# Kernel tuning notes

Measured on AMD Instinct MI355X. Metric: run time of the kernel, lower is better.

The kernel has to match this reference:

```python
import jax, jax.numpy as jnp
import numpy as np

EPS = 1e-5

def _bn(x, g, b):
    # training-mode BatchNorm1d: per-feature batch stats (biased var), affine
    mu = jnp.mean(x, 0)
    var = jnp.var(x, 0)
    return (x - mu) * jax.lax.rsqrt(var + EPS) * g + b

def _sage(x_src, x_dst, src, dst, Wl, bl, Wr):
    # PyG SAGEConv(mean): lin_l(mean_{j in N(i)} x_j) + lin_r(x_i); lin_r has no bias
    n = x_dst.shape[0]
    s = jax.ops.segment_sum(x_src[src], dst, num_segments=n)          # [N_dst, H]
    c = jax.ops.segment_sum(jnp.ones(src.shape, x_src.dtype), dst, num_segments=n)
    m = s / jnp.maximum(c, 1.0)[:, None]                              # mean aggregation; isolated nodes -> 0
    return m @ Wl + bl + x_dst @ Wr


def setup_inputs() -> dict:
    ND, NG, NS = 30000, 60000, 15000
    FD, FG, FS = 256, 128, 64
    H, O = 128, 64
    E = dict(dg=500000, gd=500000, gs=400000, sg=400000, ds=150000, sd=150000)
    keys = iter(jax.random.split(jax.random.key(0), 64))
    def nrm(shape, s=0.05):
        return jax.random.normal(next(keys), shape, jnp.float32) * s
    def ridx(n, hi):
        return jax.random.randint(next(keys), (n,), 0, hi, jnp.int32)
    inp = {
        'x_drug': nrm((ND, FD), 1.0), 'x_gene': nrm((NG, FG), 1.0), 'x_dis': nrm((NS, FS), 1.0),
        'src_dg': ridx(E['dg'], ND), 'dst_dg': ridx(E['dg'], NG),
        'src_gd': ridx(E['gd'], NG), 'dst_gd': ridx(E['gd'], ND),
        'src_gs': ridx(E['gs'], NG), 'dst_gs': ridx(E['gs'], NS),
        'src_sg': ridx(E['sg'], NS), 'dst_sg': ridx(E['sg'], NG),
        'src_ds': ridx(E['ds'], ND), 'dst_ds': ridx(E['ds'], NS),
        'src_sd': ridx(E['sd'], NS), 'dst_sd': ridx(E['sd'], ND),
        # input projections per node type
        'W_in_drug': nrm((FD, H)), 'b_in_drug': jnp.zeros((H,), jnp.float32),
        'W_in_gene': nrm((FG, H)), 'b_in_gene': jnp.zeros((H,), jnp.float32),
        'W_in_dis':  nrm((FS, H)), 'b_in_dis':  jnp.zeros((H,), jnp.float32),
        # input norms, [3 node types, H]
        'g_in': jnp.ones((3, H), jnp.float32), 'bt_in': jnp.zeros((3, H), jnp.float32),
        # SAGEConv weights: [3 layers, 6 edge types, H, H]; order: dg,gd,gs,sg,ds,sd
        'Wl': nrm((3, 6, H, H)), 'Wr': nrm((3, 6, H, H)), 'bl': jnp.zeros((3, 6, H), jnp.float32),
        # per-layer per-type norms [3 layers, 3 types, H]
        'g_conv': jnp.ones((3, 3, H), jnp.float32), 'bt_conv': jnp.zeros((3, 3, H), jnp.float32),
        'W_fin': nrm((H, O)), 'b_fin': jnp.zeros((O,), jnp.float32),
    }
    return inp


def reference(x_drug, x_gene, x_dis,
              src_dg, dst_dg, src_gd, dst_gd, src_gs, dst_gs,
              src_sg, dst_sg, src_ds, dst_ds, src_sd, dst_sd,
              W_in_drug, b_in_drug, W_in_gene, b_in_gene, W_in_dis, b_in_dis,
              g_in, bt_in, Wl, Wr, bl, g_conv, bt_conv, W_fin, b_fin):
    relu = jax.nn.relu
    # input proj + BN + ReLU (dropout in eval mode = identity)
    hd = relu(_bn(x_drug @ W_in_drug + b_in_drug, g_in[0], bt_in[0]))
    hg = relu(_bn(x_gene @ W_in_gene + b_in_gene, g_in[1], bt_in[1]))
    hs = relu(_bn(x_dis  @ W_in_dis  + b_in_dis,  g_in[2], bt_in[2]))
    for L in range(3):
        rd, rg, rs = hd, hg, hs
        # HeteroConv aggr='mean' over the two edge types hitting each dst type
        od = ( _sage(rg, rd, src_gd, dst_gd, Wl[L,1], bl[L,1], Wr[L,1])
             + _sage(rs, rd, src_sd, dst_sd, Wl[L,5], bl[L,5], Wr[L,5]) ) * 0.5
        og = ( _sage(rd, rg, src_dg, dst_dg, Wl[L,0], bl[L,0], Wr[L,0])
             + _sage(rs, rg, src_sg, dst_sg, Wl[L,3], bl[L,3], Wr[L,3]) ) * 0.5
        os_ = ( _sage(rg, rs, src_gs, dst_gs, Wl[L,2], bl[L,2], Wr[L,2])
              + _sage(rd, rs, src_ds, dst_ds, Wl[L,4], bl[L,4], Wr[L,4]) ) * 0.5
        hd = relu(_bn(od,  g_conv[L,0], bt_conv[L,0])) + rd
        hg = relu(_bn(og,  g_conv[L,1], bt_conv[L,1])) + rg
        hs = relu(_bn(os_, g_conv[L,2], bt_conv[L,2])) + rs
    return (hd @ W_fin + b_fin, hg @ W_fin + b_fin, hs @ W_fin + b_fin)
```

## Files before the change

### kernel.cpp

```cpp
#include <hip/hip_runtime.h>
#include <cstddef>
#include <cstdint>

typedef _Float16 f16;
typedef _Float16 f16x8 __attribute__((ext_vector_type(8)));
typedef float f32x4 __attribute__((ext_vector_type(4)));

constexpr int ND = 30000, NG = 60000, NS = 15000;
constexpr float BN_EPS = 1e-5f;
constexpr int NBUCK = 64;
constexpr int TBUCK = 6 * NBUCK;
constexpr int PCHUNK = 4096;

static inline int cdiv(int a, int b){ return (a + b - 1) / b; }


struct BDesc {
    const int* src[6]; const int* dst[6];
    int Ebase[7]; int shift[6]; int N[6];
    int* bCnt; int* bBase; int* bCursor;
    uint2* packed;
    int* offs[6]; int* csr[6];
};

__global__ __launch_bounds__(256) void bhist_k(BDesc bd){
    __shared__ int hist[TBUCK];
    int tid = threadIdx.x;
    for (int i = tid; i < TBUCK; i += 256) hist[i] = 0;
    __syncthreads();
    int Etot = bd.Ebase[6];
    #pragma unroll
    for (int u = 0; u < 16; u++){
        int e = blockIdx.x * PCHUNK + u * 256 + tid;
        if (e < Etot){
            int t = 0;
            #pragma unroll
            for (int i = 1; i < 6; i++) if (e >= bd.Ebase[i]) t = i;
            int d = bd.dst[t][e - bd.Ebase[t]];
            atomicAdd(&hist[t * NBUCK + (d >> bd.shift[t])], 1);
        }
    }
    __syncthreads();
    for (int i = tid; i < TBUCK; i += 256)
        if (hist[i]) atomicAdd(&bd.bCnt[i], hist[i]);
}

__global__ __launch_bounds__(512) void bscan_k(BDesc bd){
    __shared__ int sh[TBUCK];
    int tid = threadIdx.x;
    int my = (tid < TBUCK) ? bd.bCnt[tid] : 0;
    if (tid < TBUCK) sh[tid] = my;
    __syncthreads();
    for (int d = 1; d < TBUCK; d <<= 1){
        int v = (tid < TBUCK) ? sh[tid] : 0;
        int add = (tid >= d && tid < TBUCK) ? sh[tid - d] : 0;
        __syncthreads();
        if (tid < TBUCK) sh[tid] = v + add;
        __syncthreads();
    }
    if (tid < TBUCK){
        int excl = sh[tid] - my;
        bd.bBase[tid] = excl;
        bd.bCursor[tid] = excl;
    }
    if (tid == 0) bd.bBase[TBUCK] = sh[TBUCK - 1];
}

__global__ __launch_bounds__(256) void bpart_k(BDesc bd){
    __shared__ int hist[TBUCK];
    __shared__ int basesh[TBUCK];
    int tid = threadIdx.x;
    for (int i = tid; i < TBUCK; i += 256) hist[i] = 0;
    __syncthreads();
    int Etot = bd.Ebase[6];
    int mb[16], mr[16], ms[16], md[16];
    #pragma unroll
    for (int u = 0; u < 16; u++){
        int e = blockIdx.x * PCHUNK + u * 256 + tid;
        mb[u] = -1;
        if (e < Etot){
            int t = 0;
            #pragma unroll
            for (int i = 1; i < 6; i++) if (e >= bd.Ebase[i]) t = i;
            int le = e - bd.Ebase[t];
            int s = bd.src[t][le], d = bd.dst[t][le];
            int b = t * NBUCK + (d >> bd.shift[t]);
            mr[u] = atomicAdd(&hist[b], 1);
            mb[u] = b; ms[u] = s; md[u] = d;
        }
    }
    __syncthreads();
    for (int i = tid; i < TBUCK; i += 256)
        basesh[i] = hist[i] ? atomicAdd(&bd.bCursor[i], hist[i]) : 0;
    __syncthreads();
    #pragma unroll
    for (int u = 0; u < 16; u++){
        if (mb[u] >= 0){
            int pos = basesh[mb[u]] + mr[u];
            bd.packed[pos] = make_uint2((unsigned)ms[u], (unsigned)md[u]);
        }
    }
}

__global__ __launch_bounds__(256) void bucketCsr_k(BDesc bd){
    __shared__ int cnt[1024];
    __shared__ int sh[256];
    int b = blockIdx.x;
    int t = b >> 6;
    int bb = b & 63;
    int tid = threadIdx.x;
    int shift = bd.shift[t];
    int nodeBase = bb << shift;
    int Nt = bd.N[t];
    int span = 1 << shift;
    int tbase = bd.bBase[t * NBUCK];
    int eBeg = bd.bBase[b], eEnd = bd.bBase[b + 1];
    int bLocal = eBeg - tbase;
    #pragma unroll
    for (int i = 0; i < 4; i++) cnt[tid + i * 256] = 0;
    __syncthreads();
    for (int e = eBeg + tid; e < eEnd; e += 256)
        atomicAdd(&cnt[(int)bd.packed[e].y - nodeBase], 1);
    __syncthreads();
    int c0 = cnt[tid * 4], c1 = cnt[tid * 4 + 1], c2 = cnt[tid * 4 + 2], c3 = cnt[tid * 4 + 3];
    int s = c0 + c1 + c2 + c3;
    sh[tid] = s;
    __syncthreads();
    for (int d = 1; d < 256; d <<= 1){
        int v = sh[tid];
        int add = (tid >= d) ? sh[tid - d] : 0;
        __syncthreads();
        sh[tid] = v + add;
        __syncthreads();
    }
    int run = sh[tid] - s;
    int idx = tid * 4;
    int ex0 = run, ex1 = run + c0, ex2 = ex1 + c1, ex3 = ex2 + c2;
    if (idx     < span && nodeBase + idx     < Nt) bd.offs[t][nodeBase + idx]     = bLocal + ex0;
    if (idx + 1 < span && nodeBase + idx + 1 < Nt) bd.offs[t][nodeBase + idx + 1] = bLocal + ex1;
    if (idx + 2 < span && nodeBase + idx + 2 < Nt) bd.offs[t][nodeBase + idx + 2] = bLocal + ex2;
    if (idx + 3 < span && nodeBase + idx + 3 < Nt) bd.offs[t][nodeBase + idx + 3] = bLocal + ex3;
    cnt[idx] = ex0; cnt[idx + 1] = ex1; cnt[idx + 2] = ex2; cnt[idx + 3] = ex3;
    __syncthreads();
    for (int e = eBeg + tid; e < eEnd; e += 256){
        uint2 p = bd.packed[e];
        int lpos = atomicAdd(&cnt[(int)p.y - nodeBase], 1);
        bd.csr[t][bLocal + lpos] = (int)p.x;
    }
    if (bb == NBUCK - 1 && tid == 0)
        bd.offs[t][Nt] = bd.bBase[(t + 1) * NBUCK] - tbase;
}


struct WDesc {
    const float* W_in0; const float* W_in1; const float* W_in2;
    const float* W_fin; const float* Wl; const float* Wr;
    f16* Wint0; f16* Wint1; f16* Wint2; f16* Wfin_t; f16* Wcat_t;
};

__global__ __launch_bounds__(256) void weightAll_k(WDesc wd){
    int idx = blockIdx.x * 256 + threadIdx.x;
    if (idx < 32768){
        int c = idx >> 8, k = idx & 255;
        wd.Wint0[idx] = (f16)wd.W_in0[k * 128 + c];
    } else if (idx < 49152){
        int l = idx - 32768; int c = l >> 7, k = l & 127;
        wd.Wint1[l] = (f16)wd.W_in1[k * 128 + c];
    } else if (idx < 57344){
        int l = idx - 49152; int c = l >> 6, k = l & 63;
        wd.Wint2[l] = (f16)wd.W_in2[k * 128 + c];
    } else if (idx < 65536){
        int l = idx - 57344; int c = l >> 7, k = l & 127;
        wd.Wfin_t[l] = (f16)wd.W_fin[k * 64 + c];
    } else if (idx < 507904){
        int l = idx - 65536;
        int g = l / (384 * 128);
        int rem = l - g * (384 * 128);
        int c = rem / 384;
        int k = rem - c * 384;
        int L = g / 3, t = g - L * 3;
        const int e1s[3] = {1, 0, 2}, e2s[3] = {5, 3, 4};
        int e1 = e1s[t], e2 = e2s[t];
        float v;
        if (k < 128)      v = wd.Wl[(((size_t)L * 6 + e1) * 128 + k) * 128 + c];
        else if (k < 256) v = wd.Wl[(((size_t)L * 6 + e2) * 128 + (k - 128)) * 128 + c];
        else {
            int kr = k - 256;
            v = wd.Wr[(((size_t)L * 6 + e1) * 128 + kr) * 128 + c]
              + wd.Wr[(((size_t)L * 6 + e2) * 128 + kr) * 128 + c];
        }
        wd.Wcat_t[l] = (f16)v;
    }
}


struct GSeg { const int* offs; const int* csr; const uint4* h; uint4* A; int colPair4; int N; int base; };
struct GDesc { GSeg s[6]; const uint4* zrow; };

__device__ __forceinline__ f16x8 as_h8(uint4 v){
    union { uint4 u; f16x8 h; } c; c.u = v; return c.h;
}

__global__ __launch_bounds__(256) void gatherall_k(GDesc gd){
    int bid = blockIdx.x;
    int si = 0;
    #pragma unroll
    for (int t = 1; t < 6; t++) if (bid >= gd.s[t].base) si = t;
    GSeg sg = gd.s[si];
    int node = (bid - sg.base) * 16 + (threadIdx.x >> 4);
    if (node >= sg.N) return;
    int li = threadIdx.x & 15;
    int s = sg.offs[node], e = sg.offs[node + 1];
    const int* cp = sg.csr;
    const uint4* hp = sg.h;
    const uint4* zr = gd.zrow;
    f16x8 a = {};
    for (int j = s; j < e; j += 8){
        const uint4* p0 = (j + 0 < e) ? (hp + (size_t)cp[j + 0] * 16) : zr;
        const uint4* p1 = (j + 1 < e) ? (hp + (size_t)cp[j + 1] * 16) : zr;
        const uint4* p2 = (j + 2 < e) ? (hp + (size_t)cp[j + 2] * 16) : zr;
        const uint4* p3 = (j + 3 < e) ? (hp + (size_t)cp[j + 3] * 16) : zr;
        const uint4* p4 = (j + 4 < e) ? (hp + (size_t)cp[j + 4] * 16) : zr;
        const uint4* p5 = (j + 5 < e) ? (hp + (size_t)cp[j + 5] * 16) : zr;
        const uint4* p6 = (j + 6 < e) ? (hp + (size_t)cp[j + 6] * 16) : zr;
        const uint4* p7 = (j + 7 < e) ? (hp + (size_t)cp[j + 7] * 16) : zr;
        uint4 v0 = p0[li], v1 = p1[li], v2 = p2[li], v3 = p3[li];
        uint4 v4 = p4[li], v5 = p5[li], v6 = p6[li], v7 = p7[li];
        a = a + as_h8(v0); a = a + as_h8(v1); a = a + as_h8(v2); a = a + as_h8(v3);
        a = a + as_h8(v4); a = a + as_h8(v5); a = a + as_h8(v6); a = a + as_h8(v7);
    }
    float inv = (e > s) ? 1.0f / (float)(e - s) : 0.f;
    union { uint4 u; f16 h[8]; } pk;
    #pragma unroll
    for (int i = 0; i < 8; i++) pk.h[i] = (f16)((float)a[i] * inv);
    sg.A[(size_t)node * 32 + sg.colPair4 + li] = pk.u;
}


struct GemmSeg {
    const f16* A1; const f16* A2; const f16* Wt;
    const float* b1; const float* b2; void* out; float* stats;
    int lda1, lda2, ksplit, N, K, tileBase; float scale;
};
struct GemmDesc { GemmSeg s[3]; };

template<int BN, bool STATS, bool OUT16, bool A32>
__global__ __launch_bounds__(256) void gemmAll_k(GemmDesc gd){
    constexpr int CF = BN / 16;
    __shared__ f16 As[128 * 64];
    __shared__ f16 Bs[BN * 64];
    __shared__ float ssum[BN];
    __shared__ float ssq[BN];
    int bid = blockIdx.x;
    int si = 0;
    #pragma unroll
    for (int t = 1; t < 3; t++) if (bid >= gd.s[t].tileBase) si = t;
    GemmSeg sg = gd.s[si];
    int tid = threadIdx.x;
    int wv = tid >> 6, lane = tid & 63;
    int row0 = (bid - sg.tileBase) * 128;
    int N = sg.N, K = sg.K;
    if (STATS && tid < BN){ ssum[tid] = 0.f; ssq[tid] = 0.f; }

    int rsub = lane >> 3;
    int seg  = lane & 7;
    int sseg = seg ^ rsub;

    f32x4 acc[2][CF];
    #pragma unroll
    for (int rf = 0; rf < 2; rf++)
        #pragma unroll
        for (int cf = 0; cf < CF; cf++)
            acc[rf][cf] = (f32x4){0.f, 0.f, 0.f, 0.f};

    for (int k0 = 0; k0 < K; k0 += 64){
        if (A32){
            const float* Af = (const float*)sg.A1;
            int lda = sg.lda1;
            #pragma unroll
            for (int p = 0; p < 4; p++){
                int sidx = tid + p * 256;
                int r = sidx >> 3, sg8 = sidx & 7;
                int gr = row0 + r;
                int gseg = sg8 ^ (r & 7);
                float4 u0 = make_float4(0.f, 0.f, 0.f, 0.f), u1 = u0;
                if (gr < N){
                    const float* ap = Af + (size_t)gr * lda + k0 + gseg * 8;
                    u0 = *reinterpret_cast<const float4*>(ap);
                    u1 = *reinterpret_cast<const float4*>(ap + 4);
                }
                union { uint4 u; f16 h[8]; } pk;
                pk.h[0] = (f16)u0.x; pk.h[1] = (f16)u0.y; pk.h[2] = (f16)u0.z; pk.h[3] = (f16)u0.w;
                pk.h[4] = (f16)u1.x; pk.h[5] = (f16)u1.y; pk.h[6] = (f16)u1.z; pk.h[7] = (f16)u1.w;
                *reinterpret_cast<uint4*>(&As[r * 64 + sg8 * 8]) = pk.u;
            }
        } else {
            const f16* Ab; int lda, kloc;
            if (k0 < sg.ksplit){ Ab = sg.A1; lda = sg.lda1; kloc = k0; }
            else               { Ab = sg.A2; lda = sg.lda2; kloc = k0 - sg.ksplit; }
            #pragma unroll
            for (int p = 0; p < 4; p++){
                int r = wv * 32 + p * 8 + rsub;
                const f16* srca = Ab + (size_t)(row0 + r) * lda + kloc + sseg * 8;
                __builtin_amdgcn_global_load_lds(
                    (const __attribute__((address_space(1))) void*)srca,
                    (__attribute__((address_space(3))) void*)&As[(wv * 32 + p * 8) * 64],
                    16, 0, 0);
            }
        }
        #pragma unroll
        for (int p = 0; p < BN / 32; p++){
            int c0 = wv * (BN / 4) + p * 8;
            const f16* srcb = sg.Wt + (size_t)(c0 + rsub) * K + k0 + sseg * 8;
            __builtin_amdgcn_global_load_lds(
                (const __attribute__((address_space(1))) void*)srcb,
                (__attribute__((address_space(3))) void*)&Bs[c0 * 64],
                16, 0, 0);
        }
        __syncthreads();
        #pragma unroll
        for (int kf = 0; kf < 2; kf++){
            int kidx = kf * 4 + (lane >> 4);
            int ar0 = wv * 32 + (lane & 15);
            int ar1 = ar0 + 16;
            f16x8 a0 = *reinterpret_cast<const f16x8*>(&As[ar0 * 64 + ((kidx ^ (ar0 & 7)) * 8)]);
            f16x8 a1 = *reinterpret_cast<const f16x8*>(&As[ar1 * 64 + ((kidx ^ (ar1 & 7)) * 8)]);
            #pragma unroll
            for (int cf = 0; cf < CF; cf++){
                int bc = cf * 16 + (lane & 15);
                f16x8 b = *reinterpret_cast<const f16x8*>(&Bs[bc * 64 + ((kidx ^ (bc & 7)) * 8)]);
                acc[0][cf] = __builtin_amdgcn_mfma_f32_16x16x32_f16(a0, b, acc[0][cf], 0, 0, 0);
                acc[1][cf] = __builtin_amdgcn_mfma_f32_16x16x32_f16(a1, b, acc[1][cf], 0, 0, 0);
            }
        }
        __syncthreads();
    }
    int rbase = row0 + wv * 32 + ((lane >> 4) << 2);
    #pragma unroll
    for (int cf = 0; cf < CF; cf++){
        int col = cf * 16 + (lane & 15);
        float bias = 0.f;
        if (sg.b1) bias += sg.b1[col];
        if (sg.b2) bias += sg.b2[col];
        float ls = 0.f, lq = 0.f;
        #pragma unroll
        for (int rf = 0; rf < 2; rf++){
            #pragma unroll
            for (int q = 0; q < 4; q++){
                int gr = rbase + rf * 16 + q;
                if (gr < N){
                    float v = sg.scale * (acc[rf][cf][q] + bias);
                    if (OUT16) ((f16*)sg.out)[(size_t)gr * BN + col] = (f16)v;
                    else       ((float*)sg.out)[(size_t)gr * BN + col] = v;
                    ls += v; lq += v * v;
                }
            }
        }
        if (STATS){ atomicAdd(&ssum[col], ls); atomicAdd(&ssq[col], lq); }
    }
    if (STATS){
        __syncthreads();
        if (tid < BN){
            atomicAdd(&sg.stats[tid], ssum[tid]);
            atomicAdd(&sg.stats[128 + tid], ssq[tid]);
        }
    }
}


struct BnSeg { const f16* o; const float* stats; const float* g; const float* b; f16* h; int N; float invN; int residual; int idxBase; };
struct BnDesc { BnSeg s[3]; int total; };

__global__ __launch_bounds__(256) void bnAll_k(BnDesc bd){
    int idx = blockIdx.x * 256 + threadIdx.x;
    if (idx >= bd.total) return;
    int si = 0;
    #pragma unroll
    for (int t = 1; t < 3; t++) if (idx >= bd.s[t].idxBase) si = t;
    BnSeg sg = bd.s[si];
    int l = idx - sg.idxBase;
    int n = l >> 4, c8 = (l & 15) * 8;
    union { uint4 u; f16 h[8]; } ov;
    ov.u = *reinterpret_cast<const uint4*>(sg.o + (size_t)n * 128 + c8);
    float r[8];
    #pragma unroll
    for (int j = 0; j < 8; j++){
        int c = c8 + j;
        float mu  = sg.stats[c] * sg.invN;
        float var = sg.stats[128 + c] * sg.invN - mu * mu;
        float v = ((float)ov.h[j] - mu) * rsqrtf(var + BN_EPS) * sg.g[c] + sg.b[c];
        r[j] = v > 0.f ? v : 0.f;
    }
    f16* hp = sg.h + (size_t)n * 128 + c8;
    if (sg.residual){
        uint4 old = *reinterpret_cast<const uint4*>(hp);
        union { uint4 u; f16 h[8]; } ou; ou.u = old;
        #pragma unroll
        for (int j = 0; j < 8; j++) r[j] += (float)ou.h[j];
    }
    union { uint4 u; f16 h[8]; } pk;
    #pragma unroll
    for (int j = 0; j < 8; j++) pk.h[j] = (f16)r[j];
    *reinterpret_cast<uint4*>(hp) = pk.u;
}


extern "C" void kernel_launch(void* const* d_in, const int* in_sizes, int n_in,
                              void* d_out, int out_size, void* d_ws, size_t ws_size,
                              hipStream_t stream){
    const float* x_drug = (const float*)d_in[0];
    const float* x_gene = (const float*)d_in[1];
    const float* x_dis  = (const float*)d_in[2];
    const int* srcP[6] = {(const int*)d_in[3], (const int*)d_in[5], (const int*)d_in[7],
                          (const int*)d_in[9], (const int*)d_in[11], (const int*)d_in[13]};
    const int* dstP[6] = {(const int*)d_in[4], (const int*)d_in[6], (const int*)d_in[8],
                          (const int*)d_in[10], (const int*)d_in[12], (const int*)d_in[14]};
    const int  Et[6]   = {in_sizes[3], in_sizes[5], in_sizes[7], in_sizes[9], in_sizes[11], in_sizes[13]};
    const float* W_in[3] = {(const float*)d_in[15], (const float*)d_in[17], (const float*)d_in[19]};
    const float* b_in[3] = {(const float*)d_in[16], (const float*)d_in[18], (const float*)d_in[20]};
    const float* g_in  = (const float*)d_in[21];
    const float* bt_in = (const float*)d_in[22];
    const float* Wl    = (const float*)d_in[23];
    const float* Wr    = (const float*)d_in[24];
    const float* bl    = (const float*)d_in[25];
    const float* g_conv  = (const float*)d_in[26];
    const float* bt_conv = (const float*)d_in[27];
    const float* W_fin = (const float*)d_in[28];
    const float* b_fin = (const float*)d_in[29];
    float* out = (float*)d_out;

    const int Ndst_t[6]     = {NG, ND, NS, NG, NS, ND};
    const int srcT[6]       = {0, 1, 1, 2, 0, 2};
    const int dstT[6]       = {1, 0, 2, 1, 2, 0};
    const int colPair4_t[6] = {0, 0, 0, 16, 16, 16};

    const int Nn[3]  = {ND, NG, NS};
    const int Kin[3] = {256, 128, 64};
    const float* xin[3] = {x_drug, x_gene, x_dis};

    char* base = (char*)d_ws;
    size_t off = 0;
    auto alloc = [&](size_t bytes) -> char* {
        char* p = base + off; off += (bytes + 255) & ~(size_t)255; return p;
    };
    f16* h[3];  for (int t = 0; t < 3; t++) h[t]  = (f16*)alloc((size_t)Nn[t] * 128 * 2);
    f16* A[3];  for (int t = 0; t < 3; t++) A[t]  = (f16*)alloc((size_t)Nn[t] * 256 * 2);
    f16* Wint[3]; for (int t = 0; t < 3; t++) Wint[t] = (f16*)alloc((size_t)128 * Kin[t] * 2);
    f16* Wfin_t = (f16*)alloc((size_t)64 * 128 * 2);
    f16* Wcat_t = (f16*)alloc((size_t)9 * 128 * 384 * 2);
    char* oPool = alloc((size_t)(ND + NG + NS) * 128 * 2);
    f16* o[3];
    o[0] = (f16*)oPool; o[1] = o[0] + (size_t)ND * 128; o[2] = o[1] + (size_t)NG * 128;
    uint2* packed = (uint2*)oPool;
    float* stats = (float*)alloc(12 * 256 * 4);
    int* zeroPool = (int*)alloc((size_t)(TBUCK + 64) * 4);
    int* bCnt = zeroPool;
    const uint4* zrow = (const uint4*)(zeroPool + TBUCK);
    int* bBase   = (int*)alloc((TBUCK + 1) * 4);
    int* bCursor = (int*)alloc(TBUCK * 4);
    int *offs[6], *csr[6];
    for (int t = 0; t < 6; t++) offs[t] = (int*)alloc((size_t)(Ndst_t[t] + 1) * 4);
    for (int t = 0; t < 6; t++) csr[t]  = (int*)alloc((size_t)Et[t] * 4);

    hipMemsetAsync(zeroPool, 0, (size_t)(TBUCK + 64) * 4, stream);
    hipMemsetAsync(stats, 0, 12 * 256 * 4, stream);

    BDesc bd;
    {
        int ecum = 0;
        for (int t = 0; t < 6; t++){
            bd.src[t] = srcP[t]; bd.dst[t] = dstP[t];
            bd.Ebase[t] = ecum; ecum += Et[t];
            int sft = 0; while (((Ndst_t[t] - 1) >> sft) >= NBUCK) sft++;
            bd.shift[t] = sft;
            bd.N[t] = Ndst_t[t];
            bd.offs[t] = offs[t]; bd.csr[t] = csr[t];
        }
        bd.Ebase[6] = ecum;
        bd.bCnt = bCnt; bd.bBase = bBase; bd.bCursor = bCursor;
        bd.packed = packed;
    }
    int Etot = bd.Ebase[6];
    bhist_k<<<cdiv(Etot, PCHUNK), 256, 0, stream>>>(bd);
    bscan_k<<<1, 512, 0, stream>>>(bd);
    bpart_k<<<cdiv(Etot, PCHUNK), 256, 0, stream>>>(bd);
    bucketCsr_k<<<TBUCK, 256, 0, stream>>>(bd);

    WDesc wd = {W_in[0], W_in[1], W_in[2], W_fin, Wl, Wr,
                Wint[0], Wint[1], Wint[2], Wfin_t, Wcat_t};
    weightAll_k<<<cdiv(507904, 256), 256, 0, stream>>>(wd);

    int tiles[3]; for (int t = 0; t < 3; t++) tiles[t] = cdiv(Nn[t], 128);
    int tileBase[4] = {0, tiles[0], tiles[0] + tiles[1], tiles[0] + tiles[1] + tiles[2]};

    {
        GemmDesc g{};
        for (int t = 0; t < 3; t++){
            g.s[t] = {(const f16*)xin[t], (const f16*)xin[t], Wint[t], b_in[t], nullptr,
                      o[t], stats + t * 256,
                      Kin[t], Kin[t], Kin[t], Nn[t], Kin[t], tileBase[t], 1.0f};
        }
        gemmAll_k<128, true, true, true><<<tileBase[3], 256, 0, stream>>>(g);
        BnDesc bnd{}; int ib = 0;
        for (int t = 0; t < 3; t++){
            bnd.s[t] = {o[t], stats + t * 256, g_in + t * 128, bt_in + t * 128, h[t],
                        Nn[t], 1.0f / Nn[t], 0, ib};
            ib += Nn[t] * 16;
        }
        bnd.total = ib;
        bnAll_k<<<cdiv(ib, 256), 256, 0, stream>>>(bnd);
    }

    const int e1s[3] = {1, 0, 2}, e2s[3] = {5, 3, 4};
    for (int L = 0; L < 3; L++){
        GDesc gd; int bacc = 0;
        gd.zrow = zrow;
        for (int t = 0; t < 6; t++){
            gd.s[t].offs = offs[t];
            gd.s[t].csr  = csr[t];
            gd.s[t].h    = (const uint4*)h[srcT[t]];
            gd.s[t].A    = (uint4*)A[dstT[t]];
            gd.s[t].colPair4 = colPair4_t[t];
            gd.s[t].N    = Ndst_t[t];
            gd.s[t].base = bacc;
            bacc += cdiv(Ndst_t[t], 16);
        }
        gatherall_k<<<bacc, 256, 0, stream>>>(gd);
        GemmDesc g{};
        for (int t = 0; t < 3; t++){
            int e1 = e1s[t], e2 = e2s[t];
            g.s[t] = {A[t], h[t], Wcat_t + (size_t)(L * 3 + t) * 128 * 384,
                      bl + (size_t)(L * 6 + e1) * 128, bl + (size_t)(L * 6 + e2) * 128,
                      o[t], stats + (size_t)(3 + L * 3 + t) * 256,
                      256, 128, 256, Nn[t], 384, tileBase[t], 0.5f};
        }
        gemmAll_k<128, true, true, false><<<tileBase[3], 256, 0, stream>>>(g);
        BnDesc bnd{}; int ib = 0;
        for (int t = 0; t < 3; t++){
            bnd.s[t] = {o[t], stats + (size_t)(3 + L * 3 + t) * 256,
                        g_conv + (size_t)(L * 3 + t) * 128, bt_conv + (size_t)(L * 3 + t) * 128,
                        h[t], Nn[t], 1.0f / Nn[t], 1, ib};
            ib += Nn[t] * 16;
        }
        bnd.total = ib;
        bnAll_k<<<cdiv(ib, 256), 256, 0, stream>>>(bnd);
    }

    {
        int Ntot = ND + NG + NS;
        GemmDesc g{};
        g.s[0] = {h[0], h[0], Wfin_t, b_fin, nullptr, out, nullptr,
                  128, 128, 128, Ntot, 128, 0, 1.0f};
        g.s[1] = g.s[0]; g.s[1].tileBase = 0x3FFFFFFF; g.s[1].N = 0;
        g.s[2] = g.s[1];
        gemmAll_k<64, false, false, false><<<cdiv(Ntot, 128), 256, 0, stream>>>(g);
    }
}
```

Before: 540.3 us.

## Fuse graph preprocessing stages with independent work into fewer combined launches

Merges the bucket histogram with the weight conversion, the partition pass with the input-projection GEMM, and the CSR build with the input BatchNorm into three combined kernels that pick their role by block index. The separate scan kernel is removed: the last histogram block, found through an atomic done counter, does the scan. The aim is to cut launch count and let independent work share the device, which adds dependence on threadfence ordering and makes packed reuse the A[0] buffer instead of the o pool.

```diff
diff --git a/kernel.cpp b/kernel.cpp
--- a/kernel.cpp
+++ b/kernel.cpp
@@ -23,15 +23,34 @@
     int* offs[6]; int* csr[6];
 };
 
-__global__ __launch_bounds__(256) void bhist_k(BDesc bd){
+struct WDesc {
+    const float* W_in0; const float* W_in1; const float* W_in2;
+    const float* W_fin; const float* Wl; const float* Wr;
+    f16* Wint0; f16* Wint1; f16* Wint2; f16* Wfin_t; f16* Wcat_t;
+};
+
+struct GemmSeg {
+    const f16* A1; const f16* A2; const f16* Wt;
+    const float* b1; const float* b2; void* out; float* stats;
+    int lda1, lda2, ksplit, N, K, tileBase; float scale;
+};
+struct GemmDesc { GemmSeg s[3]; };
+
+struct BnSeg { const f16* o; const float* stats; const float* g; const float* b; f16* h; int N; float invN; int residual; int idxBase; };
+struct BnDesc { BnSeg s[3]; int total; };
+
+
+__device__ __forceinline__ void dev_bhist(const BDesc& bd, int bid, int H, int* done){
     __shared__ int hist[TBUCK];
+    __shared__ int psum[256];
+    __shared__ int isLast;
     int tid = threadIdx.x;
     for (int i = tid; i < TBUCK; i += 256) hist[i] = 0;
     __syncthreads();
     int Etot = bd.Ebase[6];
     #pragma unroll
     for (int u = 0; u < 16; u++){
-        int e = blockIdx.x * PCHUNK + u * 256 + tid;
+        int e = bid * PCHUNK + u * 256 + tid;
         if (e < Etot){
             int t = 0;
             #pragma unroll
@@ -43,123 +62,32 @@
     __syncthreads();
     for (int i = tid; i < TBUCK; i += 256)
         if (hist[i]) atomicAdd(&bd.bCnt[i], hist[i]);
-}
-
-__global__ __launch_bounds__(512) void bscan_k(BDesc bd){
-    __shared__ int sh[TBUCK];
-    int tid = threadIdx.x;
-    int my = (tid < TBUCK) ? bd.bCnt[tid] : 0;
-    if (tid < TBUCK) sh[tid] = my;
-    __syncthreads();
-    for (int d = 1; d < TBUCK; d <<= 1){
-        int v = (tid < TBUCK) ? sh[tid] : 0;
-        int add = (tid >= d && tid < TBUCK) ? sh[tid - d] : 0;
-        __syncthreads();
-        if (tid < TBUCK) sh[tid] = v + add;
-        __syncthreads();
-    }
-    if (tid < TBUCK){
-        int excl = sh[tid] - my;
-        bd.bBase[tid] = excl;
-        bd.bCursor[tid] = excl;
-    }
-    if (tid == 0) bd.bBase[TBUCK] = sh[TBUCK - 1];
-}
-
-__global__ __launch_bounds__(256) void bpart_k(BDesc bd){
-    __shared__ int hist[TBUCK];
-    __shared__ int basesh[TBUCK];
-    int tid = threadIdx.x;
-    for (int i = tid; i < TBUCK; i += 256) hist[i] = 0;
-    __syncthreads();
-    int Etot = bd.Ebase[6];
-    int mb[16], mr[16], ms[16], md[16];
-    #pragma unroll
-    for (int u = 0; u < 16; u++){
-        int e = blockIdx.x * PCHUNK + u * 256 + tid;
-        mb[u] = -1;
-        if (e < Etot){
-            int t = 0;
-            #pragma unroll
-            for (int i = 1; i < 6; i++) if (e >= bd.Ebase[i]) t = i;
-            int le = e - bd.Ebase[t];
-            int s = bd.src[t][le], d = bd.dst[t][le];
-            int b = t * NBUCK + (d >> bd.shift[t]);
-            mr[u] = atomicAdd(&hist[b], 1);
-            mb[u] = b; ms[u] = s; md[u] = d;
-        }
-    }
-    __syncthreads();
-    for (int i = tid; i < TBUCK; i += 256)
-        basesh[i] = hist[i] ? atomicAdd(&bd.bCursor[i], hist[i]) : 0;
-    __syncthreads();
-    #pragma unroll
-    for (int u = 0; u < 16; u++){
-        if (mb[u] >= 0){
-            int pos = basesh[mb[u]] + mr[u];
-            bd.packed[pos] = make_uint2((unsigned)ms[u], (unsigned)md[u]);
-        }
-    }
-}
-
-__global__ __launch_bounds__(256) void bucketCsr_k(BDesc bd){
-    __shared__ int cnt[1024];
-    __shared__ int sh[256];
-    int b = blockIdx.x;
-    int t = b >> 6;
-    int bb = b & 63;
-    int tid = threadIdx.x;
-    int shift = bd.shift[t];
-    int nodeBase = bb << shift;
-    int Nt = bd.N[t];
-    int span = 1 << shift;
-    int tbase = bd.bBase[t * NBUCK];
-    int eBeg = bd.bBase[b], eEnd = bd.bBase[b + 1];
-    int bLocal = eBeg - tbase;
-    #pragma unroll
-    for (int i = 0; i < 4; i++) cnt[tid + i * 256] = 0;
-    __syncthreads();
-    for (int e = eBeg + tid; e < eEnd; e += 256)
-        atomicAdd(&cnt[(int)bd.packed[e].y - nodeBase], 1);
-    __syncthreads();
-    int c0 = cnt[tid * 4], c1 = cnt[tid * 4 + 1], c2 = cnt[tid * 4 + 2], c3 = cnt[tid * 4 + 3];
-    int s = c0 + c1 + c2 + c3;
-    sh[tid] = s;
-    __syncthreads();
-    for (int d = 1; d < 256; d <<= 1){
-        int v = sh[tid];
-        int add = (tid >= d) ? sh[tid - d] : 0;
-        __syncthreads();
-        sh[tid] = v + add;
-        __syncthreads();
-    }
-    int run = sh[tid] - s;
-    int idx = tid * 4;
-    int ex0 = run, ex1 = run + c0, ex2 = ex1 + c1, ex3 = ex2 + c2;
-    if (idx     < span && nodeBase + idx     < Nt) bd.offs[t][nodeBase + idx]     = bLocal + ex0;
-    if (idx + 1 < span && nodeBase + idx + 1 < Nt) bd.offs[t][nodeBase + idx + 1] = bLocal + ex1;
-    if (idx + 2 < span && nodeBase + idx + 2 < Nt) bd.offs[t][nodeBase + idx + 2] = bLocal + ex2;
-    if (idx + 3 < span && nodeBase + idx + 3 < Nt) bd.offs[t][nodeBase + idx + 3] = bLocal + ex3;
-    cnt[idx] = ex0; cnt[idx + 1] = ex1; cnt[idx + 2] = ex2; cnt[idx + 3] = ex3;
-    __syncthreads();
-    for (int e = eBeg + tid; e < eEnd; e += 256){
-        uint2 p = bd.packed[e];
-        int lpos = atomicAdd(&cnt[(int)p.y - nodeBase], 1);
-        bd.csr[t][bLocal + lpos] = (int)p.x;
-    }
-    if (bb == NBUCK - 1 && tid == 0)
-        bd.offs[t][Nt] = bd.bBase[(t + 1) * NBUCK] - tbase;
-}
-
-
-struct WDesc {
-    const float* W_in0; const float* W_in1; const float* W_in2;
-    const float* W_fin; const float* Wl; const float* Wr;
-    f16* Wint0; f16* Wint1; f16* Wint2; f16* Wfin_t; f16* Wcat_t;
-};
-
-__global__ __launch_bounds__(256) void weightAll_k(WDesc wd){
-    int idx = blockIdx.x * 256 + threadIdx.x;
+    __threadfence();
+    if (tid == 0) isLast = (atomicAdd(done, 1) == H - 1) ? 1 : 0;
+    __syncthreads();
+    if (isLast){
+        __threadfence();
+        int i0 = tid * 2, i1 = i0 + 1;
+        int a0 = (i0 < TBUCK) ? bd.bCnt[i0] : 0;
+        int a1 = (i1 < TBUCK) ? bd.bCnt[i1] : 0;
+        int p = a0 + a1;
+        psum[tid] = p; __syncthreads();
+        for (int d = 1; d < 256; d <<= 1){
+            int v = psum[tid];
+            int add = (tid >= d) ? psum[tid - d] : 0;
+            __syncthreads();
+            psum[tid] = v + add;
+            __syncthreads();
+        }
+        int excl = psum[tid] - p;
+        if (i0 < TBUCK){ bd.bBase[i0] = excl; bd.bCursor[i0] = excl; }
+        if (i1 < TBUCK){ bd.bBase[i1] = excl + a0; bd.bCursor[i1] = excl + a0; }
+        if (tid == 255) bd.bBase[TBUCK] = psum[255];
+    }
+}
+
+__device__ __forceinline__ void dev_weight(const WDesc& wd, int bid){
+    int idx = bid * 256 + threadIdx.x;
     if (idx < 32768){
         int c = idx >> 8, k = idx & 255;
         wd.Wint0[idx] = (f16)wd.W_in0[k * 128 + c];
@@ -193,65 +121,97 @@
     }
 }
 
-
-struct GSeg { const int* offs; const int* csr; const uint4* h; uint4* A; int colPair4; int N; int base; };
-struct GDesc { GSeg s[6]; const uint4* zrow; };
-
-__device__ __forceinline__ f16x8 as_h8(uint4 v){
-    union { uint4 u; f16x8 h; } c; c.u = v; return c.h;
-}
-
-__global__ __launch_bounds__(256) void gatherall_k(GDesc gd){
-    int bid = blockIdx.x;
-    int si = 0;
-    #pragma unroll
-    for (int t = 1; t < 6; t++) if (bid >= gd.s[t].base) si = t;
-    GSeg sg = gd.s[si];
-    int node = (bid - sg.base) * 16 + (threadIdx.x >> 4);
-    if (node >= sg.N) return;
-    int li = threadIdx.x & 15;
-    int s = sg.offs[node], e = sg.offs[node + 1];
-    const int* cp = sg.csr;
-    const uint4* hp = sg.h;
-    const uint4* zr = gd.zrow;
-    f16x8 a = {};
-    for (int j = s; j < e; j += 8){
-        const uint4* p0 = (j + 0 < e) ? (hp + (size_t)cp[j + 0] * 16) : zr;
-        const uint4* p1 = (j + 1 < e) ? (hp + (size_t)cp[j + 1] * 16) : zr;
-        const uint4* p2 = (j + 2 < e) ? (hp + (size_t)cp[j + 2] * 16) : zr;
-        const uint4* p3 = (j + 3 < e) ? (hp + (size_t)cp[j + 3] * 16) : zr;
-        const uint4* p4 = (j + 4 < e) ? (hp + (size_t)cp[j + 4] * 16) : zr;
-        const uint4* p5 = (j + 5 < e) ? (hp + (size_t)cp[j + 5] * 16) : zr;
-        const uint4* p6 = (j + 6 < e) ? (hp + (size_t)cp[j + 6] * 16) : zr;
-        const uint4* p7 = (j + 7 < e) ? (hp + (size_t)cp[j + 7] * 16) : zr;
-        uint4 v0 = p0[li], v1 = p1[li], v2 = p2[li], v3 = p3[li];
-        uint4 v4 = p4[li], v5 = p5[li], v6 = p6[li], v7 = p7[li];
-        a = a + as_h8(v0); a = a + as_h8(v1); a = a + as_h8(v2); a = a + as_h8(v3);
-        a = a + as_h8(v4); a = a + as_h8(v5); a = a + as_h8(v6); a = a + as_h8(v7);
-    }
-    float inv = (e > s) ? 1.0f / (float)(e - s) : 0.f;
-    union { uint4 u; f16 h[8]; } pk;
-    #pragma unroll
-    for (int i = 0; i < 8; i++) pk.h[i] = (f16)((float)a[i] * inv);
-    sg.A[(size_t)node * 32 + sg.colPair4 + li] = pk.u;
-}
-
-
-struct GemmSeg {
-    const f16* A1; const f16* A2; const f16* Wt;
-    const float* b1; const float* b2; void* out; float* stats;
-    int lda1, lda2, ksplit, N, K, tileBase; float scale;
-};
-struct GemmDesc { GemmSeg s[3]; };
+__device__ __forceinline__ void dev_bpart(const BDesc& bd, int bid){
+    __shared__ int hist[TBUCK];
+    __shared__ int basesh[TBUCK];
+    int tid = threadIdx.x;
+    for (int i = tid; i < TBUCK; i += 256) hist[i] = 0;
+    __syncthreads();
+    int Etot = bd.Ebase[6];
+    int mb[16], mr[16], ms[16], md[16];
+    #pragma unroll
+    for (int u = 0; u < 16; u++){
+        int e = bid * PCHUNK + u * 256 + tid;
+        mb[u] = -1;
+        if (e < Etot){
+            int t = 0;
+            #pragma unroll
+            for (int i = 1; i < 6; i++) if (e >= bd.Ebase[i]) t = i;
+            int le = e - bd.Ebase[t];
+            int s = bd.src[t][le], d = bd.dst[t][le];
+            int b = t * NBUCK + (d >> bd.shift[t]);
+            mr[u] = atomicAdd(&hist[b], 1);
+            mb[u] = b; ms[u] = s; md[u] = d;
+        }
+    }
+    __syncthreads();
+    for (int i = tid; i < TBUCK; i += 256)
+        basesh[i] = hist[i] ? atomicAdd(&bd.bCursor[i], hist[i]) : 0;
+    __syncthreads();
+    #pragma unroll
+    for (int u = 0; u < 16; u++){
+        if (mb[u] >= 0){
+            int pos = basesh[mb[u]] + mr[u];
+            bd.packed[pos] = make_uint2((unsigned)ms[u], (unsigned)md[u]);
+        }
+    }
+}
+
+__device__ __forceinline__ void dev_bucketCsr(const BDesc& bd, int b){
+    __shared__ int cnt[1024];
+    __shared__ int sh[256];
+    int t = b >> 6;
+    int bb = b & 63;
+    int tid = threadIdx.x;
+    int shift = bd.shift[t];
+    int nodeBase = bb << shift;
+    int Nt = bd.N[t];
+    int span = 1 << shift;
+    int tbase = bd.bBase[t * NBUCK];
+    int eBeg = bd.bBase[b], eEnd = bd.bBase[b + 1];
+    int bLocal = eBeg - tbase;
+    #pragma unroll
+    for (int i = 0; i < 4; i++) cnt[tid + i * 256] = 0;
+    __syncthreads();
+    for (int e = eBeg + tid; e < eEnd; e += 256)
+        atomicAdd(&cnt[(int)bd.packed[e].y - nodeBase], 1);
+    __syncthreads();
+    int c0 = cnt[tid * 4], c1 = cnt[tid * 4 + 1], c2 = cnt[tid * 4 + 2], c3 = cnt[tid * 4 + 3];
+    int s = c0 + c1 + c2 + c3;
+    sh[tid] = s;
+    __syncthreads();
+    for (int d = 1; d < 256; d <<= 1){
+        int v = sh[tid];
+        int add = (tid >= d) ? sh[tid - d] : 0;
+        __syncthreads();
+        sh[tid] = v + add;
+        __syncthreads();
+    }
+    int run = sh[tid] - s;
+    int idx = tid * 4;
+    int ex0 = run, ex1 = run + c0, ex2 = ex1 + c1, ex3 = ex2 + c2;
+    if (idx     < span && nodeBase + idx     < Nt) bd.offs[t][nodeBase + idx]     = bLocal + ex0;
+    if (idx + 1 < span && nodeBase + idx + 1 < Nt) bd.offs[t][nodeBase + idx + 1] = bLocal + ex1;
+    if (idx + 2 < span && nodeBase + idx + 2 < Nt) bd.offs[t][nodeBase + idx + 2] = bLocal + ex2;
+    if (idx + 3 < span && nodeBase + idx + 3 < Nt) bd.offs[t][nodeBase + idx + 3] = bLocal + ex3;
+    cnt[idx] = ex0; cnt[idx + 1] = ex1; cnt[idx + 2] = ex2; cnt[idx + 3] = ex3;
+    __syncthreads();
+    for (int e = eBeg + tid; e < eEnd; e += 256){
+        uint2 p = bd.packed[e];
+        int lpos = atomicAdd(&cnt[(int)p.y - nodeBase], 1);
+        bd.csr[t][bLocal + lpos] = (int)p.x;
+    }
+    if (bb == NBUCK - 1 && tid == 0)
+        bd.offs[t][Nt] = bd.bBase[(t + 1) * NBUCK] - tbase;
+}
 
 template<int BN, bool STATS, bool OUT16, bool A32>
-__global__ __launch_bounds__(256) void gemmAll_k(GemmDesc gd){
+__device__ __forceinline__ void dev_gemm(const GemmDesc& gd, int bid){
     constexpr int CF = BN / 16;
     __shared__ f16 As[128 * 64];
     __shared__ f16 Bs[BN * 64];
     __shared__ float ssum[BN];
     __shared__ float ssq[BN];
-    int bid = blockIdx.x;
     int si = 0;
     #pragma unroll
     for (int t = 1; t < 3; t++) if (bid >= gd.s[t].tileBase) si = t;
@@ -367,12 +327,8 @@
     }
 }
 
-
-struct BnSeg { const f16* o; const float* stats; const float* g; const float* b; f16* h; int N; float invN; int residual; int idxBase; };
-struct BnDesc { BnSeg s[3]; int total; };
-
-__global__ __launch_bounds__(256) void bnAll_k(BnDesc bd){
-    int idx = blockIdx.x * 256 + threadIdx.x;
+__device__ __forceinline__ void dev_bn(const BnDesc& bd, int bid){
+    int idx = bid * 256 + threadIdx.x;
     if (idx >= bd.total) return;
     int si = 0;
     #pragma unroll
@@ -402,6 +358,74 @@
     #pragma unroll
     for (int j = 0; j < 8; j++) pk.h[j] = (f16)r[j];
     *reinterpret_cast<uint4*>(hp) = pk.u;
+}
+
+
+__global__ __launch_bounds__(256) void d1_k(BDesc bd, WDesc wd, int H, int* done){
+    if ((int)blockIdx.x < H) dev_bhist(bd, blockIdx.x, H, done);
+    else                     dev_weight(wd, blockIdx.x - H);
+}
+
+__global__ __launch_bounds__(256) void d2_k(BDesc bd, GemmDesc gd, int G){
+    if ((int)blockIdx.x < G) dev_gemm<128, true, true, true>(gd, blockIdx.x);
+    else                     dev_bpart(bd, blockIdx.x - G);
+}
+
+__global__ __launch_bounds__(256) void d3_k(BDesc bd, BnDesc bnd, int C){
+    if ((int)blockIdx.x < C) dev_bucketCsr(bd, blockIdx.x);
+    else                     dev_bn(bnd, blockIdx.x - C);
+}
+
+
+struct GSeg { const int* offs; const int* csr; const uint4* h; uint4* A; int colPair4; int N; int base; };
+struct GDesc { GSeg s[6]; const uint4* zrow; };
+
+__device__ __forceinline__ f16x8 as_h8(uint4 v){
+    union { uint4 u; f16x8 h; } c; c.u = v; return c.h;
+}
+
+__global__ __launch_bounds__(256) void gatherall_k(GDesc gd){
+    int bid = blockIdx.x;
+    int si = 0;
+    #pragma unroll
+    for (int t = 1; t < 6; t++) if (bid >= gd.s[t].base) si = t;
+    GSeg sg = gd.s[si];
+    int node = (bid - sg.base) * 16 + (threadIdx.x >> 4);
+    if (node >= sg.N) return;
+    int li = threadIdx.x & 15;
+    int s = sg.offs[node], e = sg.offs[node + 1];
+    const int* cp = sg.csr;
+    const uint4* hp = sg.h;
+    const uint4* zr = gd.zrow;
+    f16x8 a = {};
+    for (int j = s; j < e; j += 8){
+        const uint4* p0 = (j + 0 < e) ? (hp + (size_t)cp[j + 0] * 16) : zr;
+        const uint4* p1 = (j + 1 < e) ? (hp + (size_t)cp[j + 1] * 16) : zr;
+        const uint4* p2 = (j + 2 < e) ? (hp + (size_t)cp[j + 2] * 16) : zr;
+        const uint4* p3 = (j + 3 < e) ? (hp + (size_t)cp[j + 3] * 16) : zr;
+        const uint4* p4 = (j + 4 < e) ? (hp + (size_t)cp[j + 4] * 16) : zr;
+        const uint4* p5 = (j + 5 < e) ? (hp + (size_t)cp[j + 5] * 16) : zr;
+        const uint4* p6 = (j + 6 < e) ? (hp + (size_t)cp[j + 6] * 16) : zr;
+        const uint4* p7 = (j + 7 < e) ? (hp + (size_t)cp[j + 7] * 16) : zr;
+        uint4 v0 = p0[li], v1 = p1[li], v2 = p2[li], v3 = p3[li];
+        uint4 v4 = p4[li], v5 = p5[li], v6 = p6[li], v7 = p7[li];
+        a = a + as_h8(v0); a = a + as_h8(v1); a = a + as_h8(v2); a = a + as_h8(v3);
+        a = a + as_h8(v4); a = a + as_h8(v5); a = a + as_h8(v6); a = a + as_h8(v7);
+    }
+    float inv = (e > s) ? 1.0f / (float)(e - s) : 0.f;
+    union { uint4 u; f16 h[8]; } pk;
+    #pragma unroll
+    for (int i = 0; i < 8; i++) pk.h[i] = (f16)((float)a[i] * inv);
+    sg.A[(size_t)node * 32 + sg.colPair4 + li] = pk.u;
+}
+
+template<int BN, bool STATS, bool OUT16, bool A32>
+__global__ __launch_bounds__(256) void gemmAll_k(GemmDesc gd){
+    dev_gemm<BN, STATS, OUT16, A32>(gd, blockIdx.x);
+}
+
+__global__ __launch_bounds__(256) void bnAll_k(BnDesc bd){
+    dev_bn(bd, blockIdx.x);
 }
 
 
@@ -448,22 +472,20 @@
     f16* Wint[3]; for (int t = 0; t < 3; t++) Wint[t] = (f16*)alloc((size_t)128 * Kin[t] * 2);
     f16* Wfin_t = (f16*)alloc((size_t)64 * 128 * 2);
     f16* Wcat_t = (f16*)alloc((size_t)9 * 128 * 384 * 2);
-    char* oPool = alloc((size_t)(ND + NG + NS) * 128 * 2);
-    f16* o[3];
-    o[0] = (f16*)oPool; o[1] = o[0] + (size_t)ND * 128; o[2] = o[1] + (size_t)NG * 128;
-    uint2* packed = (uint2*)oPool;
-    float* stats = (float*)alloc(12 * 256 * 4);
-    int* zeroPool = (int*)alloc((size_t)(TBUCK + 64) * 4);
-    int* bCnt = zeroPool;
-    const uint4* zrow = (const uint4*)(zeroPool + TBUCK);
+    f16* o[3];  for (int t = 0; t < 3; t++) o[t] = (f16*)alloc((size_t)Nn[t] * 128 * 2);
+    uint2* packed = (uint2*)A[0];
+    char* zregion = alloc(2048 + 12 * 256 * 4);
+    int* bCnt = (int*)zregion;
+    const uint4* zrow = (const uint4*)(zregion + 1536);
+    int* done = (int*)(zregion + 1792);
+    float* stats = (float*)(zregion + 2048);
     int* bBase   = (int*)alloc((TBUCK + 1) * 4);
     int* bCursor = (int*)alloc(TBUCK * 4);
     int *offs[6], *csr[6];
     for (int t = 0; t < 6; t++) offs[t] = (int*)alloc((size_t)(Ndst_t[t] + 1) * 4);
     for (int t = 0; t < 6; t++) csr[t]  = (int*)alloc((size_t)Et[t] * 4);
 
-    hipMemsetAsync(zeroPool, 0, (size_t)(TBUCK + 64) * 4, stream);
-    hipMemsetAsync(stats, 0, 12 * 256 * 4, stream);
+    hipMemsetAsync(zregion, 0, 2048 + 12 * 256 * 4, stream);
 
     BDesc bd;
     {
@@ -481,35 +503,33 @@
         bd.packed = packed;
     }
     int Etot = bd.Ebase[6];
-    bhist_k<<<cdiv(Etot, PCHUNK), 256, 0, stream>>>(bd);
-    bscan_k<<<1, 512, 0, stream>>>(bd);
-    bpart_k<<<cdiv(Etot, PCHUNK), 256, 0, stream>>>(bd);
-    bucketCsr_k<<<TBUCK, 256, 0, stream>>>(bd);
-
+    int H = cdiv(Etot, PCHUNK);
+    int Wb = cdiv(507904, 256);
     WDesc wd = {W_in[0], W_in[1], W_in[2], W_fin, Wl, Wr,
                 Wint[0], Wint[1], Wint[2], Wfin_t, Wcat_t};
-    weightAll_k<<<cdiv(507904, 256), 256, 0, stream>>>(wd);
 
     int tiles[3]; for (int t = 0; t < 3; t++) tiles[t] = cdiv(Nn[t], 128);
     int tileBase[4] = {0, tiles[0], tiles[0] + tiles[1], tiles[0] + tiles[1] + tiles[2]};
-
-    {
-        GemmDesc g{};
-        for (int t = 0; t < 3; t++){
-            g.s[t] = {(const f16*)xin[t], (const f16*)xin[t], Wint[t], b_in[t], nullptr,
-                      o[t], stats + t * 256,
-                      Kin[t], Kin[t], Kin[t], Nn[t], Kin[t], tileBase[t], 1.0f};
-        }
-        gemmAll_k<128, true, true, true><<<tileBase[3], 256, 0, stream>>>(g);
-        BnDesc bnd{}; int ib = 0;
-        for (int t = 0; t < 3; t++){
-            bnd.s[t] = {o[t], stats + t * 256, g_in + t * 128, bt_in + t * 128, h[t],
-                        Nn[t], 1.0f / Nn[t], 0, ib};
-            ib += Nn[t] * 16;
-        }
-        bnd.total = ib;
-        bnAll_k<<<cdiv(ib, 256), 256, 0, stream>>>(bnd);
-    }
+    int G = tileBase[3];
+
+    d1_k<<<H + Wb, 256, 0, stream>>>(bd, wd, H, done);
+
+    GemmDesc gIn{};
+    for (int t = 0; t < 3; t++){
+        gIn.s[t] = {(const f16*)xin[t], (const f16*)xin[t], Wint[t], b_in[t], nullptr,
+                    o[t], stats + t * 256,
+                    Kin[t], Kin[t], Kin[t], Nn[t], Kin[t], tileBase[t], 1.0f};
+    }
+    d2_k<<<G + H, 256, 0, stream>>>(bd, gIn, G);
+
+    BnDesc bnIn{}; int ibIn = 0;
+    for (int t = 0; t < 3; t++){
+        bnIn.s[t] = {o[t], stats + t * 256, g_in + t * 128, bt_in + t * 128, h[t],
+                     Nn[t], 1.0f / Nn[t], 0, ibIn};
+        ibIn += Nn[t] * 16;
+    }
+    bnIn.total = ibIn;
+    d3_k<<<TBUCK + cdiv(ibIn, 256), 256, 0, stream>>>(bd, bnIn, TBUCK);
 
     const int e1s[3] = {1, 0, 2}, e2s[3] = {5, 3, 4};
     for (int L = 0; L < 3; L++){
@@ -534,7 +554,7 @@
                       o[t], stats + (size_t)(3 + L * 3 + t) * 256,
                       256, 128, 256, Nn[t], 384, tileBase[t], 0.5f};
         }
-        gemmAll_k<128, true, true, false><<<tileBase[3], 256, 0, stream>>>(g);
+        gemmAll_k<128, true, true, false><<<G, 256, 0, stream>>>(g);
         BnDesc bnd{}; int ib = 0;
         for (int t = 0; t < 3; t++){
             bnd.s[t] = {o[t], stats + (size_t)(3 + L * 3 + t) * 256,
```

Measured after the change: 548.2 us. Within noise of the previous version (+1.5%).
